# Kernel optimization log

Hardware: AMD Instinct MI355X
Metric: run time of the kernel (lower is better)

## Reference

```python
import jax, jax.numpy as jnp
import numpy as np

# Model constants (match init_kwargs)
B, V, NUM_NODES, NUM_RELS = 32, 20, 4000, 400
EMB, HID, L, N, E, OUT = 128, 128, 3, 32000, 256000, 128
DECAY = 0.03
EPS = 0.0  # self_attn eps, not trained


def setup_inputs() -> dict:
    key = jax.random.key(0)
    ks = jax.random.split(key, 20)
    s = 0.02
    return {
        "node_ids": jax.random.randint(ks[0], (N,), 0, NUM_NODES),
        "rel_ids": jax.random.randint(ks[1], (E,), 0, NUM_RELS),
        "edge_index": jax.random.randint(ks[2], (2, E), 0, N),
        "batch": jnp.sort(jax.random.randint(ks[3], (N,), 0, B)),
        "visit_node": jax.random.uniform(ks[4], (B, V, NUM_NODES), dtype=jnp.float32),
        "ehr_nodes": jax.random.uniform(ks[5], (B, NUM_NODES), dtype=jnp.float32),
        "node_emb": jax.random.normal(ks[6], (NUM_NODES, EMB), dtype=jnp.float32) * s,
        "rel_emb": jax.random.normal(ks[7], (NUM_RELS, EMB), dtype=jnp.float32) * s,
        "lin_w": jax.random.normal(ks[8], (HID, EMB), dtype=jnp.float32) * s,
        "lin_b": jnp.zeros((HID,), jnp.float32),
        "alpha_w": jax.random.normal(ks[9], (L, NUM_NODES, NUM_NODES), dtype=jnp.float32) * 0.002,
        "alpha_b": jnp.zeros((L, NUM_NODES), jnp.float32),
        "beta_w": jax.random.normal(ks[10], (L, 1, NUM_NODES), dtype=jnp.float32) * s,
        "beta_b": jnp.zeros((L, 1), jnp.float32),
        "wr_w": jax.random.normal(ks[11], (L, 1, HID), dtype=jnp.float32) * s,
        "wr_b": jnp.zeros((L, 1), jnp.float32),
        "nn_w": jax.random.normal(ks[12], (L, HID, HID), dtype=jnp.float32) * s,
        "nn_b": jnp.zeros((L, HID), jnp.float32),
        "mlp_w": jax.random.normal(ks[13], (OUT, 2 * HID), dtype=jnp.float32) * s,
        "mlp_b": jnp.zeros((OUT,), jnp.float32),
    }


def reference(node_ids, rel_ids, edge_index, batch, visit_node, ehr_nodes,
              node_emb, rel_emb, lin_w, lin_b, alpha_w, alpha_b, beta_w, beta_b,
              wr_w, wr_b, nn_w, nn_b, mlp_w, mlp_b):
    # visit decay weights lambda_j: (1, V, 1)
    lambda_j = jnp.exp(DECAY * (V - jnp.arange(V, dtype=jnp.float32))).reshape(1, V, 1)

    x = node_emb[node_ids] @ lin_w.T + lin_b          # (N, HID)
    edge_attr = rel_emb[rel_ids] @ lin_w.T + lin_b    # (E, HID)
    src, dst = edge_index[0], edge_index[1]
    nid_src = node_ids[src]
    b_src = batch[src]

    for l in range(L):
        # alpha: softmax over visit dim, (B, V, NUM_NODES)
        alpha = jax.nn.softmax(
            jnp.einsum('bvn,mn->bvm', visit_node, alpha_w[l]) + alpha_b[l], axis=1)
        # beta: (B, V, 1) with visit decay
        beta = jnp.tanh(
            jnp.einsum('bvn,on->bvo', visit_node, beta_w[l]) + beta_b[l]) * lambda_j
        attn = jnp.sum(alpha * beta, axis=1)          # (B, NUM_NODES)
        e_attn = attn[b_src, nid_src][:, None]        # (E, 1) per-edge attention

        # BiAttentionGNNConv message: relu(x_j * attn + W_R(edge_attr) * edge_attr)
        w_rel = edge_attr @ wr_w[l].T + wr_b[l]       # (E, 1)
        msg = jax.nn.relu(x[src] * e_attn + w_rel * edge_attr)
        agg = jax.ops.segment_sum(msg, dst, num_segments=N)  # scatter-add aggregate
        out = agg + (1.0 + EPS) * x                   # eps residual
        x = jax.nn.relu(out @ nn_w[l].T + nn_b[l])    # conv.nn Linear + outer relu

    # graph-level patient embedding: global mean pool over batch
    counts = jnp.maximum(
        jax.ops.segment_sum(jnp.ones((N, 1), x.dtype), batch, num_segments=B), 1.0)
    x_graph = jax.ops.segment_sum(x, batch, num_segments=B) / counts  # (B, HID)

    # node-level patient embedding: ehr multihot average of node embeddings
    x_node = (ehr_nodes @ node_emb) / jnp.sum(ehr_nodes, axis=1, keepdims=True)
    x_node = x_node @ lin_w.T + lin_b                 # (B, HID)

    logits = jnp.concatenate([x_graph, x_node], axis=1) @ mlp_w.T + mlp_b
    return logits
```

## Files before the change

### kernel.cpp

```cpp
#include <hip/hip_runtime.h>

namespace {

constexpr int kNodes = 4000;
constexpr int kRels  = 400;
constexpr int kB     = 32;
constexpr int kV     = 20;
constexpr int kN     = 32000;
constexpr int kE     = 256000;
constexpr int kH     = 128;
constexpr int kL     = 3;
constexpr int kMPad  = 4096;
constexpr int kKW    = 4000;
constexpr int kBV    = kB * kV;
constexpr int kNB    = 32;
constexpr int kChunk = kE / kNB;
constexpr int kHalf  = 16000;

typedef __attribute__((ext_vector_type(8))) short bf16x8;
typedef __attribute__((ext_vector_type(4))) float f32x4;

__device__ inline unsigned short f2bf(float f){
  unsigned int u = __float_as_uint(f);
  u += 0x7FFFu + ((u >> 16) & 1u);
  return (unsigned short)(u >> 16);
}

__device__ inline void gload_lds16(const unsigned short* g, unsigned short* l){
  __builtin_amdgcn_global_load_lds(
      (const __attribute__((address_space(1))) unsigned int*)(g),
      (__attribute__((address_space(3))) unsigned int*)(l),
      16, 0, 0);
}


__global__ void transpose_kernel(const float* __restrict__ lin_w, const float* __restrict__ nn_w,
                                 float* __restrict__ lin_wT, float* __restrict__ nn_wT){
  int m = blockIdx.x;
  const float* in = (m == 0) ? lin_w : nn_w + (size_t)(m-1)*kH*kH;
  float* out      = (m == 0) ? lin_wT : nn_wT + (size_t)(m-1)*kH*kH;
  for (int i = threadIdx.x; i < kH*kH; i += blockDim.x){
    int r = i >> 7, c = i & (kH-1);
    out[c*kH + r] = in[i];
  }
}

__global__ __launch_bounds__(128) void proj_kernel(const float* __restrict__ node_emb,
    const float* __restrict__ rel_emb, const float* __restrict__ lin_wT,
    const float* __restrict__ lin_b, float* __restrict__ emb_lin, float* __restrict__ rel_lin){
  int row = blockIdx.x;
  const float* src; float* dst;
  if (row < kNodes){ src = node_emb + (size_t)row*kH; dst = emb_lin + (size_t)row*kH; }
  else             { src = rel_emb + (size_t)(row-kNodes)*kH; dst = rel_lin + (size_t)(row-kNodes)*kH; }
  __shared__ float rs[kH];
  int h = threadIdx.x;
  rs[h] = src[h];
  __syncthreads();
  float acc = lin_b[h];
#pragma unroll 8
  for (int k = 0; k < kH; k++) acc = fmaf(rs[k], lin_wT[k*kH + h], acc);
  dst[h] = acc;
}

__global__ void gather_x0_kernel(const int* __restrict__ node_ids,
                                 const float* __restrict__ emb_lin, float* __restrict__ x,
                                 unsigned short* __restrict__ xbf){
  int idx = blockIdx.x*256 + threadIdx.x;
  if (idx < kN*kH){
    int i = idx >> 7, c = idx & (kH-1);
    float v = emb_lin[(size_t)node_ids[i]*kH + c];
    x[idx] = v;
    xbf[idx] = f2bf(v);
  }
}

__global__ __launch_bounds__(128) void relterm_kernel(const float* __restrict__ rel_lin,
    const float* __restrict__ wr_w, const float* __restrict__ wr_b, float* __restrict__ relterm){
  int l = blockIdx.x / kRels, r = blockIdx.x % kRels;
  int t = threadIdx.x;
  float rl = rel_lin[(size_t)r*kH + t];
  __shared__ float red[kH];
  red[t] = rl * wr_w[l*kH + t];
  __syncthreads();
  for (int o = 64; o > 0; o >>= 1){
    if (t < o) red[t] += red[t+o];
    __syncthreads();
  }
  float w = red[0] + wr_b[l];
  relterm[((size_t)l*kRels + r)*kH + t] = w * rl;
}


__global__ __launch_bounds__(256) void csr_hist_kernel(const int* __restrict__ dst,
    unsigned short* __restrict__ rank, unsigned int* __restrict__ hpart){
  __shared__ unsigned int hb[kHalf];
  int p = blockIdx.x;
  int base = blockIdx.y * kHalf;
  int t = threadIdx.x;
  for (int i = t; i < kHalf; i += 256) hb[i] = 0u;
  __syncthreads();
  for (int i = t; i < kChunk; i += 256){
    int e = p*kChunk + i;
    int d = dst[e];
    int rel = d - base;
    if ((unsigned)rel < (unsigned)kHalf){
      rank[e] = (unsigned short)atomicAdd(&hb[rel], 1u);
    }
  }
  __syncthreads();
  for (int i = t; i < kHalf; i += 256)
    hpart[(size_t)p*kN + base + i] = hb[i];
}

__global__ __launch_bounds__(256) void csr_col_kernel(unsigned int* __restrict__ hpart,
    int* __restrict__ deg){
  int bin = blockIdx.x*256 + threadIdx.x;
  if (bin >= kN) return;
  unsigned int s = 0;
#pragma unroll
  for (int p = 0; p < kNB; p++){
    size_t idx = (size_t)p*kN + bin;
    unsigned int v = hpart[idx];
    hpart[idx] = s;
    s += v;
  }
  deg[bin] = (int)s;
}

__global__ __launch_bounds__(256) void scanA_kernel(const int* __restrict__ deg,
    int* __restrict__ starts, int* __restrict__ bsum){
  __shared__ int buf[256];
  int gid = blockIdx.x*256 + threadIdx.x;
  int t = threadIdx.x;
  int v = (gid < kN) ? deg[gid] : 0;
  buf[t] = v;
  __syncthreads();
  for (int o = 1; o < 256; o <<= 1){
    int add = (t >= o) ? buf[t-o] : 0;
    __syncthreads();
    buf[t] += add;
    __syncthreads();
  }
  if (gid < kN) starts[gid] = buf[t] - v;
  if (t == 255) bsum[blockIdx.x] = buf[255];
}

__global__ __launch_bounds__(128) void scanB_kernel(const int* __restrict__ bsum,
    int* __restrict__ boffs, int nblk){
  __shared__ int buf[128];
  int t = threadIdx.x;
  int v = (t < nblk) ? bsum[t] : 0;
  buf[t] = v;
  __syncthreads();
  for (int o = 1; o < 128; o <<= 1){
    int add = (t >= o) ? buf[t-o] : 0;
    __syncthreads();
    buf[t] += add;
    __syncthreads();
  }
  if (t < nblk) boffs[t] = buf[t] - v;
}

__global__ __launch_bounds__(256) void scanC_kernel(int* __restrict__ starts,
    const int* __restrict__ boffs){
  int gid = blockIdx.x*256 + threadIdx.x;
  if (gid < kN) starts[gid] += boffs[blockIdx.x];
  if (gid == kN-1) starts[kN] = kE;
}

__global__ __launch_bounds__(256) void csr_place_kernel(const int* __restrict__ dst,
    const int* __restrict__ src, const int* __restrict__ rel_ids,
    const int* __restrict__ starts, const unsigned int* __restrict__ colOff,
    const unsigned short* __restrict__ rank,
    int* __restrict__ src_perm, int* __restrict__ rel_perm){
  int blk = blockIdx.x;
  int p = blk >> 2;
  for (int i = threadIdx.x; i < 2000; i += 256){
    int e = blk*2000 + i;
    int d = dst[e];
    int pos = starts[d] + (int)colOff[(size_t)p*kN + d] + (int)rank[e];
    src_perm[pos] = src[e];
    rel_perm[pos] = rel_ids[e];
  }
}

__global__ void ub_kernel(const int* __restrict__ batch, int* __restrict__ ub){
  int j = threadIdx.x;
  if (j > kB) return;
  int lo = 0, hi = kN;
  while (lo < hi){
    int mid = (lo + hi) >> 1;
    if (batch[mid] < j) lo = mid + 1; else hi = mid;
  }
  ub[j] = lo;
}


__global__ void cvt_visit_kernel(const float* __restrict__ visit, unsigned short* __restrict__ out){
  int i = blockIdx.x*256 + threadIdx.x;
  if (i >= kBV*(kKW/8)) return;
  int row = i / (kKW/8);
  int col = (i - row*(kKW/8)) * 8;
  const float* p = visit + (size_t)row*kKW + col;
  const float4 a = *reinterpret_cast<const float4*>(p);
  const float4 b = *reinterpret_cast<const float4*>(p + 4);
  unsigned short r[8] = {f2bf(a.x),f2bf(a.y),f2bf(a.z),f2bf(a.w),
                         f2bf(b.x),f2bf(b.y),f2bf(b.z),f2bf(b.w)};
  *reinterpret_cast<uint4*>(out + (size_t)row*kKW + col) = *reinterpret_cast<uint4*>(r);
}

__global__ void cvtW_kernel(const float* __restrict__ W, unsigned short* __restrict__ out){
  int i = blockIdx.x*256 + threadIdx.x;
  constexpr int perL = kMPad*(kKW/8);
  if (i >= kL*perL) return;
  int l = i / perL;
  int rem = i - l*perL;
  int row = rem / (kKW/8);
  int col = (rem - row*(kKW/8)) * 8;
  unsigned short r[8];
  if (row < kNodes){
    const float* p = W + (size_t)l*kNodes*kNodes + (size_t)row*kKW + col;
    const float4 a = *reinterpret_cast<const float4*>(p);
    const float4 b = *reinterpret_cast<const float4*>(p + 4);
    r[0]=f2bf(a.x); r[1]=f2bf(a.y); r[2]=f2bf(a.z); r[3]=f2bf(a.w);
    r[4]=f2bf(b.x); r[5]=f2bf(b.y); r[6]=f2bf(b.z); r[7]=f2bf(b.w);
  } else {
    for (int q = 0; q < 8; q++) r[q] = 0;
  }
  *reinterpret_cast<uint4*>(out + (size_t)l*kMPad*kKW + (size_t)row*kKW + col)
      = *reinterpret_cast<uint4*>(r);
}

__global__ __launch_bounds__(256) void gemm_bt_bf16(const unsigned short* __restrict__ A,
    const unsigned short* __restrict__ Ball, float* __restrict__ Sbase){
  __shared__ unsigned short As[2][128*32];
  __shared__ unsigned short Bs[2][128*32];
  int wg = (blockIdx.x & 7)*120 + (blockIdx.x >> 3);
  int lz = wg / 160;
  int rem = wg - lz*160;
  int bn = rem / 5;
  int bm = rem - bn*5;
  int l = lz >> 1, z = lz & 1;
  const unsigned short* B = Ball + (size_t)l*kMPad*kKW;
  float* C = Sbase + (size_t)lz*kBV*kMPad;
  int tile0 = z ? 63 : 0;
  int nt    = z ? 62 : 63;

  int t = threadIdx.x;
  int lane = t & 63, wave = t >> 6;
  int wm = (wave >> 1) * 64, wn = (wave & 1) * 64;
  int r = lane & 15, g = lane >> 4;

  int ri = lane >> 2, s = lane & 3;
  int koff = ((s ^ ((ri >> 1) & 3)) << 3);
  const unsigned short* Ag = A + (size_t)(bm*128 + wave*32 + ri)*kKW + tile0*32 + koff;
  const unsigned short* Bg = B + (size_t)(bn*128 + wave*32 + ri)*kKW + tile0*32 + koff;
  const size_t rstep = (size_t)16*kKW;

  f32x4 acc[4][4];
#pragma unroll
  for (int i = 0; i < 4; i++)
#pragma unroll
    for (int j = 0; j < 4; j++) acc[i][j] = f32x4{0.f,0.f,0.f,0.f};

  auto STAGE = [&](int buf, int ts){
    const unsigned short* a = Ag + ts*32;
    const unsigned short* b = Bg + ts*32;
    gload_lds16(a,         &As[buf][(wave*32     )*32]);
    gload_lds16(a + rstep, &As[buf][(wave*32 + 16)*32]);
    gload_lds16(b,         &Bs[buf][(wave*32     )*32]);
    gload_lds16(b + rstep, &Bs[buf][(wave*32 + 16)*32]);
  };

  STAGE(0, 0);
  for (int ts = 0; ts < nt; ts++){
    int cur = ts & 1;
    __syncthreads();
    if (ts + 1 < nt) STAGE(cur ^ 1, ts + 1);
    bf16x8 af[4], bf[4];
#pragma unroll
    for (int i = 0; i < 4; i++){
      int arow = wm + i*16 + r;
      int brow = wn + i*16 + r;
      af[i] = *reinterpret_cast<const bf16x8*>(
          &As[cur][arow*32 + ((g ^ ((arow >> 1) & 3)) << 3)]);
      bf[i] = *reinterpret_cast<const bf16x8*>(
          &Bs[cur][brow*32 + ((g ^ ((brow >> 1) & 3)) << 3)]);
    }
#pragma unroll
    for (int i = 0; i < 4; i++)
#pragma unroll
      for (int j = 0; j < 4; j++)
        acc[i][j] = __builtin_amdgcn_mfma_f32_16x16x32_bf16(af[i], bf[j], acc[i][j], 0, 0, 0);
  }
#pragma unroll
  for (int i = 0; i < 4; i++)
#pragma unroll
    for (int j = 0; j < 4; j++){
      int row = bm*128 + wm + i*16 + g*4;
      int col = bn*128 + wn + j*16 + r;
#pragma unroll
      for (int q = 0; q < 4; q++)
        C[(size_t)(row + q)*kMPad + col] = acc[i][j][q];
    }
}

__global__ __launch_bounds__(256) void beta_all_kernel(const float* __restrict__ visit,
    const float* __restrict__ beta_w, const float* __restrict__ beta_b,
    float* __restrict__ beta){
  int wid = (blockIdx.x*256 + threadIdx.x) >> 6;
  int lane = threadIdx.x & 63;
  if (wid >= kL*kBV) return;
  int l = wid / kBV, bv = wid - l*kBV;
  const float* row = visit + (size_t)bv*kNodes;
  const float* bw = beta_w + (size_t)l*kNodes;
  float s = 0.f;
  for (int k = lane; k < kNodes; k += 64) s = fmaf(row[k], bw[k], s);
#pragma unroll
  for (int o = 32; o > 0; o >>= 1) s += __shfl_down(s, o);
  if (lane == 0){
    int v = bv % kV;
    float lam = __expf(0.03f * (float)(kV - v));
    beta[wid] = tanhf(s + beta_b[l]) * lam;
  }
}

__global__ __launch_bounds__(256) void attn_kernel(const float* __restrict__ S,
    const float* __restrict__ beta, float* __restrict__ attn){
  int idx = blockIdx.x*256 + threadIdx.x;
  if (idx >= kL*kB*kNodes) return;
  int l = idx / (kB*kNodes);
  int rem = idx - l*(kB*kNodes);
  int b = rem / kNodes;
  int m = rem - b*kNodes;
  const float* S0 = S + (size_t)(l*2)*kBV*kMPad + (size_t)b*kV*kMPad + m;
  const float* S1 = S0 + (size_t)kBV*kMPad;
  float vals[kV];
  float mx = -1e30f;
#pragma unroll
  for (int v = 0; v < kV; v++){
    float s = S0[(size_t)v*kMPad] + S1[(size_t)v*kMPad];
    vals[v] = s; mx = fmaxf(mx, s);
  }
  float se = 0.f, ws = 0.f;
  const float* bp = beta + l*kBV + b*kV;
#pragma unroll
  for (int v = 0; v < kV; v++){ float e = __expf(vals[v] - mx); se += e; ws = fmaf(e, bp[v], ws); }
  attn[idx] = ws / se;
}

__global__ void att_e_kernel(const int* __restrict__ src_perm, const int* __restrict__ batch,
    const int* __restrict__ node_ids, const float* __restrict__ attn,
    float* __restrict__ att_e){
  int idx = blockIdx.x*256 + threadIdx.x;
  if (idx >= kL*kE) return;
  int l = idx / kE, p = idx - l*kE;
  int s = src_perm[p];
  att_e[idx] = attn[(size_t)l*kB*kNodes + (size_t)batch[s]*kNodes + node_ids[s]];
}


__global__ __launch_bounds__(512) void aggnn_kernel(const int* __restrict__ starts,
    const int* __restrict__ src_perm, const int* __restrict__ rel_perm,
    const float* __restrict__ att_e_l, const float* __restrict__ relterm_l,
    const unsigned short* __restrict__ xbf_in, unsigned short* __restrict__ xbf_out,
    float* __restrict__ x, const float* __restrict__ nn_wT_l, const float* __restrict__ nn_b_l){
  __shared__ float rows[8][kH];
  int t = threadIdx.x;
  int wv = t >> 6, lane = t & 63;
  int node = blockIdx.x*8 + wv;
  int p0 = starts[node], p1 = starts[node+1];
  int c = lane*2;
  float a0 = 0.f, a1 = 0.f;
  for (int p = p0; p < p1; p++){
    float at = att_e_l[p];
    int s = src_perm[p];
    int rel = rel_perm[p];
    unsigned int xv = *reinterpret_cast<const unsigned int*>(&xbf_in[(size_t)s*kH + c]);
    float2 rt = *reinterpret_cast<const float2*>(&relterm_l[(size_t)rel*kH + c]);
    float x0 = __uint_as_float(xv << 16);
    float x1 = __uint_as_float(xv & 0xFFFF0000u);
    float m0 = fmaf(x0, at, rt.x); m0 = m0 > 0.f ? m0 : 0.f;
    float m1 = fmaf(x1, at, rt.y); m1 = m1 > 0.f ? m1 : 0.f;
    a0 += m0; a1 += m1;
  }
  size_t gi = (size_t)node*kH + c;
  rows[wv][c]   = a0 + x[gi];
  rows[wv][c+1] = a1 + x[gi+1];
  __syncthreads();
  int cc = t & 127;
  int r0 = (t >> 7) * 2;
  float acc0 = 0.f, acc1 = 0.f;
#pragma unroll 8
  for (int k = 0; k < kH; k++){
    float w = nn_wT_l[k*kH + cc];
    acc0 = fmaf(rows[r0  ][k], w, acc0);
    acc1 = fmaf(rows[r0+1][k], w, acc1);
  }
  float b = nn_b_l[cc];
  float o0 = fmaxf(acc0 + b, 0.f);
  float o1 = fmaxf(acc1 + b, 0.f);
  size_t n0 = (size_t)(blockIdx.x*8 + r0)*kH + cc;
  x[n0]        = o0;  xbf_out[n0]        = f2bf(o0);
  x[n0 + kH]   = o1;  xbf_out[n0 + kH]   = f2bf(o1);
}


__global__ __launch_bounds__(128) void pool_part_kernel(const float* __restrict__ x,
    const int* __restrict__ ub, float* __restrict__ pp){
  int s = blockIdx.x, b = blockIdx.y, c = threadIdx.x;
  int lo = ub[b], len = ub[b+1] - lo;
  int i0 = lo + (int)(((long long)len * s) >> 3);
  int i1 = lo + (int)(((long long)len * (s+1)) >> 3);
  float acc = 0.f;
  for (int i = i0; i < i1; i++) acc += x[(size_t)i*kH + c];
  pp[(size_t)(b*8 + s)*kH + c] = acc;
}

__global__ __launch_bounds__(128) void xnode1_kernel(const float* __restrict__ ehr,
    const float* __restrict__ node_emb, float* __restrict__ pn, float* __restrict__ ps){
  int s = blockIdx.x, b = blockIdx.y, c = threadIdx.x;
  int n0 = s * (kNodes/8), n1 = n0 + (kNodes/8);
  float acc = 0.f, es = 0.f;
  for (int n = n0; n < n1; n++){
    float e = ehr[(size_t)b*kNodes + n];
    es += e;
    acc = fmaf(e, node_emb[(size_t)n*kH + c], acc);
  }
  pn[(size_t)(b*8 + s)*kH + c] = acc;
  if (c == 0) ps[b*8 + s] = es;
}

__global__ __launch_bounds__(128) void readout_kernel(const float* __restrict__ pp,
    const int* __restrict__ ub, const float* __restrict__ pn, const float* __restrict__ ps,
    const float* __restrict__ lin_wT, const float* __restrict__ lin_b,
    const float* __restrict__ mlp_w, const float* __restrict__ mlp_b,
    float* __restrict__ out){
  int b = blockIdx.x, h = threadIdx.x;
  __shared__ float v[2*kH];
  __shared__ float ts[kH];
  float s = 0.f;
#pragma unroll
  for (int q = 0; q < 8; q++) s += pp[(size_t)(b*8 + q)*kH + h];
  int len = ub[b+1] - ub[b]; if (len < 1) len = 1;
  v[h] = s / (float)len;
  float acc = 0.f, es = 0.f;
#pragma unroll
  for (int q = 0; q < 8; q++){
    acc += pn[(size_t)(b*8 + q)*kH + h];
    es  += ps[b*8 + q];
  }
  ts[h] = acc / es;
  __syncthreads();
  float r = lin_b[h];
#pragma unroll 8
  for (int k = 0; k < kH; k++) r = fmaf(ts[k], lin_wT[k*kH + h], r);
  v[kH + h] = r;
  __syncthreads();
  float o = mlp_b[h];
#pragma unroll 8
  for (int k = 0; k < 2*kH; k++) o = fmaf(v[k], mlp_w[(size_t)h*2*kH + k], o);
  out[b*kH + h] = o;
}

}

extern "C" void kernel_launch(void* const* d_in, const int* in_sizes, int n_in,
                              void* d_out, int out_size, void* d_ws, size_t ws_size,
                              hipStream_t stream){
  const int*   node_ids = (const int*)d_in[0];
  const int*   rel_ids  = (const int*)d_in[1];
  const int*   e_src    = (const int*)d_in[2];
  const int*   e_dst    = e_src + kE;
  const int*   batch    = (const int*)d_in[3];
  const float* visit    = (const float*)d_in[4];
  const float* ehr      = (const float*)d_in[5];
  const float* node_emb = (const float*)d_in[6];
  const float* rel_emb  = (const float*)d_in[7];
  const float* lin_w    = (const float*)d_in[8];
  const float* lin_b    = (const float*)d_in[9];
  const float* alpha_w  = (const float*)d_in[10];
  const float* beta_w   = (const float*)d_in[12];
  const float* beta_b   = (const float*)d_in[13];
  const float* wr_w     = (const float*)d_in[14];
  const float* wr_b     = (const float*)d_in[15];
  const float* nn_w     = (const float*)d_in[16];
  const float* nn_b     = (const float*)d_in[17];
  const float* mlp_w    = (const float*)d_in[18];
  const float* mlp_b    = (const float*)d_in[19];
  float* out = (float*)d_out;

  char* w = (char*)d_ws;
  auto alloc = [&](size_t bytes)->char*{
    char* p = w; w += (bytes + 255) & ~(size_t)255; return p;
  };
  int*   starts = (int*)  alloc((size_t)(kN+1)*4);
  int*   deg    = (int*)  alloc((size_t)kN*4);
  int*   bsum   = (int*)  alloc(256*4);
  int*   boffs  = (int*)  alloc(256*4);
  int*   ub     = (int*)  alloc((kB+1)*4);
  int*   src_perm = (int*)alloc((size_t)kE*4);
  int*   rel_perm = (int*)alloc((size_t)kE*4);
  unsigned short* rank = (unsigned short*)alloc((size_t)kE*2);
  unsigned int* hpart  = (unsigned int*)alloc((size_t)kNB*kN*4);
  float* embLin = (float*)alloc((size_t)kNodes*kH*4);
  float* relLin = (float*)alloc((size_t)kRels*kH*4);
  float* relterm= (float*)alloc((size_t)kL*kRels*kH*4);
  float* linwT  = (float*)alloc((size_t)kH*kH*4);
  float* nnwT   = (float*)alloc((size_t)kL*kH*kH*4);
  float* x      = (float*)alloc((size_t)kN*kH*4);
  unsigned short* xbfA = (unsigned short*)alloc((size_t)kN*kH*2);
  unsigned short* xbfB = (unsigned short*)alloc((size_t)kN*kH*2);
  unsigned short* visitbf = (unsigned short*)alloc((size_t)kBV*kKW*2);
  unsigned short* awbf    = (unsigned short*)alloc((size_t)kL*kMPad*kKW*2);
  float* S      = (float*)alloc((size_t)kL*2*kBV*kMPad*4);
  float* attn   = (float*)alloc((size_t)kL*kB*kNodes*4);
  float* att_e  = (float*)alloc((size_t)kL*kE*4);
  float* beta   = (float*)alloc((size_t)kL*kBV*4);
  float* pp     = (float*)alloc((size_t)kB*8*kH*4);
  float* pn     = (float*)alloc((size_t)kB*8*kH*4);
  float* ps     = (float*)alloc((size_t)kB*8*4);
  if ((size_t)(w - (char*)d_ws) > ws_size) return;

  transpose_kernel<<<4, 256, 0, stream>>>(lin_w, nn_w, linwT, nnwT);
  proj_kernel<<<kNodes + kRels, 128, 0, stream>>>(node_emb, rel_emb, linwT, lin_b, embLin, relLin);
  gather_x0_kernel<<<(kN*kH)/256, 256, 0, stream>>>(node_ids, embLin, x, xbfA);
  relterm_kernel<<<kL*kRels, 128, 0, stream>>>(relLin, wr_w, wr_b, relterm);

  csr_hist_kernel<<<dim3(kNB, 2), 256, 0, stream>>>(e_dst, rank, hpart);
  csr_col_kernel<<<(kN+255)/256, 256, 0, stream>>>(hpart, deg);
  scanA_kernel<<<(kN+255)/256, 256, 0, stream>>>(deg, starts, bsum);
  scanB_kernel<<<1, 128, 0, stream>>>(bsum, boffs, (kN+255)/256);
  scanC_kernel<<<(kN+255)/256, 256, 0, stream>>>(starts, boffs);
  csr_place_kernel<<<128, 256, 0, stream>>>(e_dst, e_src, rel_ids, starts, hpart, rank,
                                            src_perm, rel_perm);
  ub_kernel<<<1, 64, 0, stream>>>(batch, ub);

  cvt_visit_kernel<<<(kBV*(kKW/8) + 255)/256, 256, 0, stream>>>(visit, visitbf);
  beta_all_kernel<<<kL*kBV/4, 256, 0, stream>>>(visit, beta_w, beta_b, beta);
  cvtW_kernel<<<(kL*kMPad*(kKW/8) + 255)/256, 256, 0, stream>>>(alpha_w, awbf);
  gemm_bt_bf16<<<960, 256, 0, stream>>>(visitbf, awbf, S);
  attn_kernel<<<(kL*kB*kNodes + 255)/256, 256, 0, stream>>>(S, beta, attn);
  att_e_kernel<<<(kL*kE + 255)/256, 256, 0, stream>>>(src_perm, batch, node_ids, attn, att_e);

  unsigned short* xin = xbfA;
  unsigned short* xout = xbfB;
  for (int l = 0; l < kL; l++){
    aggnn_kernel<<<kN/8, 512, 0, stream>>>(starts, src_perm, rel_perm,
        att_e + (size_t)l*kE, relterm + (size_t)l*kRels*kH,
        xin, xout, x, nnwT + (size_t)l*kH*kH, nn_b + (size_t)l*kH);
    unsigned short* tmp = xin; xin = xout; xout = tmp;
  }

  pool_part_kernel<<<dim3(8, kB), 128, 0, stream>>>(x, ub, pp);
  xnode1_kernel<<<dim3(8, kB), 128, 0, stream>>>(ehr, node_emb, pn, ps);
  readout_kernel<<<kB, 128, 0, stream>>>(pp, ub, pn, ps, linwT, lin_b, mlp_w, mlp_b, out);
}
```

Measured before the change: 593.4 us.

## Fuse alpha_w fp32-to-bf16 conversion into GEMM B-tile staging

Removes the separate cvtW kernel that converted all three alpha weight matrices (about 192 MB fp32 read, 98 MB bf16 written) and instead has the GEMM load fp32 alpha rows into registers, convert with packed bf16 instructions, and write swizzled tiles to LDS after the MFMAs. This cuts a full extra memory round-trip for the large weight tensor. In exchange, B loads now go through registers with manual LDS stores and edge masking, which adds register pressure and VALU work inside the GEMM loop, and each B tile is read as fp32 (twice the bytes) by every block that uses it.

```diff
diff --git a/kernel.cpp b/kernel.cpp
--- a/kernel.cpp
+++ b/kernel.cpp
@@ -33,6 +33,12 @@
       16, 0, 0);
 }
 
+__device__ inline unsigned int cvt_pk_bf16(float lo, float hi){
+  unsigned int r;
+  asm("v_cvt_pk_bf16_f32 %0, %1, %2" : "=v"(r) : "v"(lo), "v"(hi));
+  return r;
+}
+
 
 __global__ void transpose_kernel(const float* __restrict__ lin_w, const float* __restrict__ nn_w,
                                  float* __restrict__ lin_wT, float* __restrict__ nn_wT){
@@ -209,30 +215,8 @@
   *reinterpret_cast<uint4*>(out + (size_t)row*kKW + col) = *reinterpret_cast<uint4*>(r);
 }
 
-__global__ void cvtW_kernel(const float* __restrict__ W, unsigned short* __restrict__ out){
-  int i = blockIdx.x*256 + threadIdx.x;
-  constexpr int perL = kMPad*(kKW/8);
-  if (i >= kL*perL) return;
-  int l = i / perL;
-  int rem = i - l*perL;
-  int row = rem / (kKW/8);
-  int col = (rem - row*(kKW/8)) * 8;
-  unsigned short r[8];
-  if (row < kNodes){
-    const float* p = W + (size_t)l*kNodes*kNodes + (size_t)row*kKW + col;
-    const float4 a = *reinterpret_cast<const float4*>(p);
-    const float4 b = *reinterpret_cast<const float4*>(p + 4);
-    r[0]=f2bf(a.x); r[1]=f2bf(a.y); r[2]=f2bf(a.z); r[3]=f2bf(a.w);
-    r[4]=f2bf(b.x); r[5]=f2bf(b.y); r[6]=f2bf(b.z); r[7]=f2bf(b.w);
-  } else {
-    for (int q = 0; q < 8; q++) r[q] = 0;
-  }
-  *reinterpret_cast<uint4*>(out + (size_t)l*kMPad*kKW + (size_t)row*kKW + col)
-      = *reinterpret_cast<uint4*>(r);
-}
-
 __global__ __launch_bounds__(256) void gemm_bt_bf16(const unsigned short* __restrict__ A,
-    const unsigned short* __restrict__ Ball, float* __restrict__ Sbase){
+    const float* __restrict__ alpha, float* __restrict__ Sbase){
   __shared__ unsigned short As[2][128*32];
   __shared__ unsigned short Bs[2][128*32];
   int wg = (blockIdx.x & 7)*120 + (blockIdx.x >> 3);
@@ -241,7 +225,7 @@
   int bn = rem / 5;
   int bm = rem - bn*5;
   int l = lz >> 1, z = lz & 1;
-  const unsigned short* B = Ball + (size_t)l*kMPad*kKW;
+  const float* B = alpha + (size_t)l*kNodes*kNodes;
   float* C = Sbase + (size_t)lz*kBV*kMPad;
   int tile0 = z ? 63 : 0;
   int nt    = z ? 62 : 63;
@@ -254,44 +238,78 @@
   int ri = lane >> 2, s = lane & 3;
   int koff = ((s ^ ((ri >> 1) & 3)) << 3);
   const unsigned short* Ag = A + (size_t)(bm*128 + wave*32 + ri)*kKW + tile0*32 + koff;
-  const unsigned short* Bg = B + (size_t)(bn*128 + wave*32 + ri)*kKW + tile0*32 + koff;
   const size_t rstep = (size_t)16*kKW;
 
+  int browLoc = wave*32 + (lane >> 1);
+  int brow = bn*128 + browLoc;
+  bool bvalid = brow < kNodes;
+  int h = lane & 1;
+  const float* Bg = B + (size_t)(bvalid ? brow : 0)*kKW + tile0*32 + h*16;
+  int bx = (browLoc >> 1) & 3;
+
   f32x4 acc[4][4];
 #pragma unroll
   for (int i = 0; i < 4; i++)
 #pragma unroll
     for (int j = 0; j < 4; j++) acc[i][j] = f32x4{0.f,0.f,0.f,0.f};
 
-  auto STAGE = [&](int buf, int ts){
+  float4 bq0, bq1, bq2, bq3;
+  auto STAGE_B_LOAD = [&](int ts){
+    const float* b = Bg + ts*32;
+    if (bvalid){
+      bq0 = *reinterpret_cast<const float4*>(b);
+      bq1 = *reinterpret_cast<const float4*>(b + 4);
+      bq2 = *reinterpret_cast<const float4*>(b + 8);
+      bq3 = *reinterpret_cast<const float4*>(b + 12);
+    } else {
+      bq0 = bq1 = bq2 = bq3 = float4{0.f,0.f,0.f,0.f};
+    }
+  };
+  auto STAGE_B_WRITE = [&](int buf){
+    unsigned int w0 = cvt_pk_bf16(bq0.x, bq0.y);
+    unsigned int w1 = cvt_pk_bf16(bq0.z, bq0.w);
+    unsigned int w2 = cvt_pk_bf16(bq1.x, bq1.y);
+    unsigned int w3 = cvt_pk_bf16(bq1.z, bq1.w);
+    unsigned int w4 = cvt_pk_bf16(bq2.x, bq2.y);
+    unsigned int w5 = cvt_pk_bf16(bq2.z, bq2.w);
+    unsigned int w6 = cvt_pk_bf16(bq3.x, bq3.y);
+    unsigned int w7 = cvt_pk_bf16(bq3.z, bq3.w);
+    unsigned short* base = &Bs[buf][browLoc*32];
+    *reinterpret_cast<uint4*>(base + ((((h<<1)    ) ^ bx) << 3)) = uint4{w0,w1,w2,w3};
+    *reinterpret_cast<uint4*>(base + ((((h<<1) + 1) ^ bx) << 3)) = uint4{w4,w5,w6,w7};
+  };
+  auto STAGE_A = [&](int buf, int ts){
     const unsigned short* a = Ag + ts*32;
-    const unsigned short* b = Bg + ts*32;
     gload_lds16(a,         &As[buf][(wave*32     )*32]);
     gload_lds16(a + rstep, &As[buf][(wave*32 + 16)*32]);
-    gload_lds16(b,         &Bs[buf][(wave*32     )*32]);
-    gload_lds16(b + rstep, &Bs[buf][(wave*32 + 16)*32]);
   };
 
-  STAGE(0, 0);
+  STAGE_B_LOAD(0);
+  STAGE_A(0, 0);
+  STAGE_B_WRITE(0);
   for (int ts = 0; ts < nt; ts++){
     int cur = ts & 1;
     __syncthreads();
-    if (ts + 1 < nt) STAGE(cur ^ 1, ts + 1);
+    if (ts + 1 < nt){
+      STAGE_B_LOAD(ts + 1);
+      STAGE_A(cur ^ 1, ts + 1);
+    }
     bf16x8 af[4], bf[4];
 #pragma unroll
     for (int i = 0; i < 4; i++){
       int arow = wm + i*16 + r;
-      int brow = wn + i*16 + r;
+      int brw  = wn + i*16 + r;
       af[i] = *reinterpret_cast<const bf16x8*>(
           &As[cur][arow*32 + ((g ^ ((arow >> 1) & 3)) << 3)]);
       bf[i] = *reinterpret_cast<const bf16x8*>(
-          &Bs[cur][brow*32 + ((g ^ ((brow >> 1) & 3)) << 3)]);
+          &Bs[cur][brw*32 + ((g ^ ((brw >> 1) & 3)) << 3)]);
     }
 #pragma unroll
     for (int i = 0; i < 4; i++)
 #pragma unroll
       for (int j = 0; j < 4; j++)
         acc[i][j] = __builtin_amdgcn_mfma_f32_16x16x32_bf16(af[i], bf[j], acc[i][j], 0, 0, 0);
+    if (ts + 1 < nt) STAGE_B_WRITE(cur ^ 1);
   }
 #pragma unroll
   for (int i = 0; i < 4; i++)
@@ -512,7 +530,6 @@
   unsigned short* xbfA = (unsigned short*)alloc((size_t)kN*kH*2);
   unsigned short* xbfB = (unsigned short*)alloc((size_t)kN*kH*2);
   unsigned short* visitbf = (unsigned short*)alloc((size_t)kBV*kKW*2);
-  unsigned short* awbf    = (unsigned short*)alloc((size_t)kL*kMPad*kKW*2);
   float* S      = (float*)alloc((size_t)kL*2*kBV*kMPad*4);
   float* attn   = (float*)alloc((size_t)kL*kB*kNodes*4);
   float* att_e  = (float*)alloc((size_t)kL*kE*4);
@@ -538,8 +555,7 @@
 
   cvt_visit_kernel<<<(kBV*(kKW/8) + 255)/256, 256, 0, stream>>>(visit, visitbf);
   beta_all_kernel<<<kL*kBV/4, 256, 0, stream>>>(visit, beta_w, beta_b, beta);
-  cvtW_kernel<<<(kL*kMPad*(kKW/8) + 255)/256, 256, 0, stream>>>(alpha_w, awbf);
-  gemm_bt_bf16<<<960, 256, 0, stream>>>(visitbf, awbf, S);
+  gemm_bt_bf16<<<960, 256, 0, stream>>>(visitbf, alpha_w, S);
   attn_kernel<<<(kL*kB*kNodes + 255)/256, 256, 0, stream>>>(S, beta, attn);
   att_e_kernel<<<(kL*kE + 255)/256, 256, 0, stream>>>(src_perm, batch, node_ids, attn, att_e);
 
```

Result: slower. 764.5 us (+28.8%).

## Fuse visit conversion with beta dots, store GEMM scores as bf16, prefetch edges

Applied to the files above, without the earlier changes.

Merges the visit-to-bf16 conversion and the three beta dot products into one kernel, so the visit tensor is read once instead of four times. The GEMM now writes its split-K partial scores as bf16 rather than fp32, which halves the traffic for the S buffer and for attn_kernel's reads of it. The aggregation loop software-prefetches the next edge's attention value, source features and relation term to hide gather latency. Storing scores in bf16 loses precision in the softmax logits, and the prefetch adds registers and extra guarded loads.

```diff
diff --git a/kernel.cpp b/kernel.cpp
--- a/kernel.cpp
+++ b/kernel.cpp
@@ -25,6 +25,9 @@
   u += 0x7FFFu + ((u >> 16) & 1u);
   return (unsigned short)(u >> 16);
 }
+__device__ inline float bf2f(unsigned short u){
+  return __uint_as_float(((unsigned int)u) << 16);
+}
 
 __device__ inline void gload_lds16(const unsigned short* g, unsigned short* l){
   __builtin_amdgcn_global_load_lds(
@@ -196,17 +199,42 @@
 }
 
 
-__global__ void cvt_visit_kernel(const float* __restrict__ visit, unsigned short* __restrict__ out){
-  int i = blockIdx.x*256 + threadIdx.x;
-  if (i >= kBV*(kKW/8)) return;
-  int row = i / (kKW/8);
-  int col = (i - row*(kKW/8)) * 8;
-  const float* p = visit + (size_t)row*kKW + col;
-  const float4 a = *reinterpret_cast<const float4*>(p);
-  const float4 b = *reinterpret_cast<const float4*>(p + 4);
-  unsigned short r[8] = {f2bf(a.x),f2bf(a.y),f2bf(a.z),f2bf(a.w),
-                         f2bf(b.x),f2bf(b.y),f2bf(b.z),f2bf(b.w)};
-  *reinterpret_cast<uint4*>(out + (size_t)row*kKW + col) = *reinterpret_cast<uint4*>(r);
+__global__ __launch_bounds__(256) void visit_prep_kernel(const float* __restrict__ visit,
+    const float* __restrict__ beta_w, const float* __restrict__ beta_b,
+    unsigned short* __restrict__ visitbf, float* __restrict__ beta){
+  int bv = blockIdx.x;
+  int t = threadIdx.x;
+  const float* row = visit + (size_t)bv*kKW;
+  unsigned short* outr = visitbf + (size_t)bv*kKW;
+  float d0 = 0.f, d1 = 0.f, d2 = 0.f;
+  for (int i = t; i < kKW/4; i += 256){
+    float4 v = *reinterpret_cast<const float4*>(row + i*4);
+    unsigned int lo = ((unsigned int)f2bf(v.y) << 16) | f2bf(v.x);
+    unsigned int hi = ((unsigned int)f2bf(v.w) << 16) | f2bf(v.z);
+    *reinterpret_cast<uint2*>(outr + i*4) = uint2{lo, hi};
+    float4 w0 = *reinterpret_cast<const float4*>(beta_w + i*4);
+    float4 w1 = *reinterpret_cast<const float4*>(beta_w + kKW + i*4);
+    float4 w2 = *reinterpret_cast<const float4*>(beta_w + 2*kKW + i*4);
+    d0 = fmaf(v.x,w0.x, fmaf(v.y,w0.y, fmaf(v.z,w0.z, fmaf(v.w,w0.w, d0))));
+    d1 = fmaf(v.x,w1.x, fmaf(v.y,w1.y, fmaf(v.z,w1.z, fmaf(v.w,w1.w, d1))));
+    d2 = fmaf(v.x,w2.x, fmaf(v.y,w2.y, fmaf(v.z,w2.z, fmaf(v.w,w2.w, d2))));
+  }
+#pragma unroll
+  for (int o = 32; o > 0; o >>= 1){
+    d0 += __shfl_down(d0, o);
+    d1 += __shfl_down(d1, o);
+    d2 += __shfl_down(d2, o);
+  }
+  __shared__ float part[3][4];
+  int wv = t >> 6, ln = t & 63;
+  if (ln == 0){ part[0][wv] = d0; part[1][wv] = d1; part[2][wv] = d2; }
+  __syncthreads();
+  if (t < 3){
+    float s = part[t][0] + part[t][1] + part[t][2] + part[t][3];
+    int v = bv % kV;
+    float lam = __expf(0.03f * (float)(kV - v));
+    beta[t*kBV + bv] = tanhf(s + beta_b[t]) * lam;
+  }
 }
 
 __global__ void cvtW_kernel(const float* __restrict__ W, unsigned short* __restrict__ out){
@@ -232,7 +260,7 @@
 }
 
 __global__ __launch_bounds__(256) void gemm_bt_bf16(const unsigned short* __restrict__ A,
-    const unsigned short* __restrict__ Ball, float* __restrict__ Sbase){
+    const unsigned short* __restrict__ Ball, unsigned short* __restrict__ Sbase){
   __shared__ unsigned short As[2][128*32];
   __shared__ unsigned short Bs[2][128*32];
   int wg = (blockIdx.x & 7)*120 + (blockIdx.x >> 3);
@@ -242,7 +270,7 @@
   int bm = rem - bn*5;
   int l = lz >> 1, z = lz & 1;
   const unsigned short* B = Ball + (size_t)l*kMPad*kKW;
-  float* C = Sbase + (size_t)lz*kBV*kMPad;
+  unsigned short* C = Sbase + (size_t)lz*kBV*kMPad;
   int tile0 = z ? 63 : 0;
   int nt    = z ? 62 : 63;
 
@@ -301,31 +329,11 @@
       int col = bn*128 + wn + j*16 + r;
 #pragma unroll
       for (int q = 0; q < 4; q++)
-        C[(size_t)(row + q)*kMPad + col] = acc[i][j][q];
+        C[(size_t)(row + q)*kMPad + col] = f2bf(acc[i][j][q]);
     }
 }
 
-__global__ __launch_bounds__(256) void beta_all_kernel(const float* __restrict__ visit,
-    const float* __restrict__ beta_w, const float* __restrict__ beta_b,
-    float* __restrict__ beta){
-  int wid = (blockIdx.x*256 + threadIdx.x) >> 6;
-  int lane = threadIdx.x & 63;
-  if (wid >= kL*kBV) return;
-  int l = wid / kBV, bv = wid - l*kBV;
-  const float* row = visit + (size_t)bv*kNodes;
-  const float* bw = beta_w + (size_t)l*kNodes;
-  float s = 0.f;
-  for (int k = lane; k < kNodes; k += 64) s = fmaf(row[k], bw[k], s);
-#pragma unroll
-  for (int o = 32; o > 0; o >>= 1) s += __shfl_down(s, o);
-  if (lane == 0){
-    int v = bv % kV;
-    float lam = __expf(0.03f * (float)(kV - v));
-    beta[wid] = tanhf(s + beta_b[l]) * lam;
-  }
-}
-
-__global__ __launch_bounds__(256) void attn_kernel(const float* __restrict__ S,
+__global__ __launch_bounds__(256) void attn_kernel(const unsigned short* __restrict__ S,
     const float* __restrict__ beta, float* __restrict__ attn){
   int idx = blockIdx.x*256 + threadIdx.x;
   if (idx >= kL*kB*kNodes) return;
@@ -333,13 +341,13 @@
   int rem = idx - l*(kB*kNodes);
   int b = rem / kNodes;
   int m = rem - b*kNodes;
-  const float* S0 = S + (size_t)(l*2)*kBV*kMPad + (size_t)b*kV*kMPad + m;
-  const float* S1 = S0 + (size_t)kBV*kMPad;
+  const unsigned short* S0 = S + (size_t)(l*2)*kBV*kMPad + (size_t)b*kV*kMPad + m;
+  const unsigned short* S1 = S0 + (size_t)kBV*kMPad;
   float vals[kV];
   float mx = -1e30f;
 #pragma unroll
   for (int v = 0; v < kV; v++){
-    float s = S0[(size_t)v*kMPad] + S1[(size_t)v*kMPad];
+    float s = bf2f(S0[(size_t)v*kMPad]) + bf2f(S1[(size_t)v*kMPad]);
     vals[v] = s; mx = fmaxf(mx, s);
   }
   float se = 0.f, ws = 0.f;
@@ -372,17 +380,32 @@
   int p0 = starts[node], p1 = starts[node+1];
   int c = lane*2;
   float a0 = 0.f, a1 = 0.f;
+
+  float at_c = 0.f;
+  unsigned int xv_c = 0u;
+  float2 rt_c = float2{0.f, 0.f};
+  if (p0 < p1){
+    int s0 = src_perm[p0], r0 = rel_perm[p0];
+    at_c = att_e_l[p0];
+    xv_c = *reinterpret_cast<const unsigned int*>(&xbf_in[(size_t)s0*kH + c]);
+    rt_c = *reinterpret_cast<const float2*>(&relterm_l[(size_t)r0*kH + c]);
+  }
   for (int p = p0; p < p1; p++){
-    float at = att_e_l[p];
-    int s = src_perm[p];
-    int rel = rel_perm[p];
-    unsigned int xv = *reinterpret_cast<const unsigned int*>(&xbf_in[(size_t)s*kH + c]);
-    float2 rt = *reinterpret_cast<const float2*>(&relterm_l[(size_t)rel*kH + c]);
-    float x0 = __uint_as_float(xv << 16);
-    float x1 = __uint_as_float(xv & 0xFFFF0000u);
-    float m0 = fmaf(x0, at, rt.x); m0 = m0 > 0.f ? m0 : 0.f;
-    float m1 = fmaf(x1, at, rt.y); m1 = m1 > 0.f ? m1 : 0.f;
+    float at_n = 0.f;
+    unsigned int xv_n = 0u;
+    float2 rt_n = float2{0.f, 0.f};
+    if (p + 1 < p1){
+      int sn = src_perm[p+1], rn = rel_perm[p+1];
+      at_n = att_e_l[p+1];
+      xv_n = *reinterpret_cast<const unsigned int*>(&xbf_in[(size_t)sn*kH + c]);
+      rt_n = *reinterpret_cast<const float2*>(&relterm_l[(size_t)rn*kH + c]);
+    }
+    float x0 = __uint_as_float(xv_c << 16);
+    float x1 = __uint_as_float(xv_c & 0xFFFF0000u);
+    float m0 = fmaf(x0, at_c, rt_c.x); m0 = m0 > 0.f ? m0 : 0.f;
+    float m1 = fmaf(x1, at_c, rt_c.y); m1 = m1 > 0.f ? m1 : 0.f;
     a0 += m0; a1 += m1;
+    at_c = at_n; xv_c = xv_n; rt_c = rt_n;
   }
   size_t gi = (size_t)node*kH + c;
   rows[wv][c]   = a0 + x[gi];
@@ -513,7 +536,7 @@
   unsigned short* xbfB = (unsigned short*)alloc((size_t)kN*kH*2);
   unsigned short* visitbf = (unsigned short*)alloc((size_t)kBV*kKW*2);
   unsigned short* awbf    = (unsigned short*)alloc((size_t)kL*kMPad*kKW*2);
-  float* S      = (float*)alloc((size_t)kL*2*kBV*kMPad*4);
+  unsigned short* S       = (unsigned short*)alloc((size_t)kL*2*kBV*kMPad*2);
   float* attn   = (float*)alloc((size_t)kL*kB*kNodes*4);
   float* att_e  = (float*)alloc((size_t)kL*kE*4);
   float* beta   = (float*)alloc((size_t)kL*kBV*4);
@@ -536,8 +559,7 @@
                                             src_perm, rel_perm);
   ub_kernel<<<1, 64, 0, stream>>>(batch, ub);
 
-  cvt_visit_kernel<<<(kBV*(kKW/8) + 255)/256, 256, 0, stream>>>(visit, visitbf);
-  beta_all_kernel<<<kL*kBV/4, 256, 0, stream>>>(visit, beta_w, beta_b, beta);
+  visit_prep_kernel<<<kBV, 256, 0, stream>>>(visit, beta_w, beta_b, visitbf, beta);
   cvtW_kernel<<<(kL*kMPad*(kKW/8) + 255)/256, 256, 0, stream>>>(alpha_w, awbf);
   gemm_bt_bf16<<<960, 256, 0, stream>>>(visitbf, awbf, S);
   attn_kernel<<<(kL*kB*kNodes + 255)/256, 256, 0, stream>>>(S, beta, attn);
```

Measured after the change: 559.2 us. -5.8%, faster.
